# Performance work log

Measured on AMD Instinct MI355X. Metric: run time of the kernel, lower is better.

## Reference

```python
import jax, jax.numpy as jnp
import numpy as np

DIM = 2048


def setup_inputs() -> dict:
    key = jax.random.key(0)
    k1, k2 = jax.random.split(key)
    skew_kernel = jax.random.normal(k1, (DIM, DIM), dtype=jnp.float32) * 0.01
    dt = jax.random.uniform(k2, (8, 256), dtype=jnp.float32)  # [batch, time]
    return {"skew_kernel": skew_kernel, "dt": dt}


def reference(skew_kernel, dt):
    # Build strictly skew-symmetric A from the upper triangle of the kernel
    K = jnp.triu(skew_kernel, 1)
    A = K - K.T                                  # [dim, dim], A^T = -A
    # H = i*A is Hermitian -> real eigenvalues L_real, unitary V
    H = (1j * A).astype(jnp.complex64)
    L_real, V = jnp.linalg.eigh(H)               # L_real: [dim], V: [dim, dim]
    L = (-1j) * L_real.astype(jnp.complex64)     # purely imaginary spectrum of A
    V_inv = V.conj().T                           # unitary inverse
    # dt broadcasting per original: ndim==2 -> [..., None]; ndim==1 -> [-1,1,1]
    if dt.ndim == 2:
        dt_cast = dt[:, :, None]
    elif dt.ndim == 1:
        dt_cast = dt.reshape(-1, 1, 1)
    else:
        dt_cast = dt[..., None]
    evo_diag = jnp.exp(L[None, None, :] * dt_cast.astype(jnp.complex64))  # [B, T, dim]
    return V, V_inv, evo_diag
```

## Files before the change

kernel.cpp:

```cpp
#include <hip/hip_runtime.h>
#include <math.h>

#define DN 2048
#define LEAF 16
#define NLEAVES 128
#define NB 64
#define SPLITK 32
#define EPSF 5.9604645e-08f
#define SAFMINF 1.17549435e-38f

typedef float2 cplx;

struct Ctl {
  float orgnrm;
  int K;
  int ctot[4];
  float rho;
  int nrot;
  int n12, n23;
};

__device__ __forceinline__ cplx mkc(float x, float y){ cplx c; c.x=x; c.y=y; return c; }
__device__ __forceinline__ cplx cmul(cplx a, cplx b){ return mkc(a.x*b.x - a.y*b.y, a.x*b.y + a.y*b.x); }
__device__ __forceinline__ cplx cconj(cplx a){ return mkc(a.x, -a.y); }
__device__ __forceinline__ cplx cadd(cplx a, cplx b){ return mkc(a.x+b.x, a.y+b.y); }
__device__ __forceinline__ cplx cinv(cplx b){
  if (fabsf(b.x) >= fabsf(b.y)) { float r = b.y/b.x; float den = b.x + b.y*r; return mkc(1.f/den, -r/den); }
  else { float r = b.x/b.y; float den = b.x*r + b.y; return mkc(r/den, -1.f/den); }
}

__global__ void k_zeroCnt(int* cnt){ if (threadIdx.x==0) *cnt = 0; }

__global__ void k_buildH_t(const float* sk, cplx* AH){
  __shared__ float tA[32][33], tB[32][33];
  int C0 = blockIdx.x*32, R0 = blockIdx.y*32;
  int tx = threadIdx.x & 31, ty = threadIdx.x >> 5;
  for (int p=0;p<4;p++){
    int ry = ty + 8*p;
    tA[ry][tx] = sk[(size_t)(R0+ry)*DN + C0+tx];
    tB[ry][tx] = sk[(size_t)(C0+ry)*DN + R0+tx];
  }
  __syncthreads();
  for (int p=0;p<4;p++){
    int cy = ty + 8*p;
    int r = R0 + tx, c = C0 + cy;
    float im;
    if (r > c) im = -tB[cy][tx];
    else if (r < c) im = tA[tx][cy];
    else im = 0.f;
    AH[(size_t)c*DN + r] = mkc(copysignf(0.f, im), im);
  }
}

__global__ void k_gemv3(cplx* AH, cplx* wpart, float* ssqpart,
                        cplx* dp, cplx* pa, cplx* a0copy, cplx* scl,
                        cplx* tauA, float* e, int* cnt, int j, int m, int chunk){
  __shared__ float rx[256], ry[256];
  __shared__ int slast;
  __shared__ cplx s_ssc;
  __shared__ int s_do;
  int t = threadIdx.x;
  int b = blockIdx.x, s = blockIdx.y;
  int i = b*256 + t;
  cplx* colr = AH + (size_t)j*DN;
  cplx* x = colr + (j+2);
  int cc0 = s*chunk, cc1 = cc0+chunk; if (cc1 > m-1) cc1 = m-1;
  if (cc0 > m-1) cc0 = m-1;
  if (b == 0){
    float ss = 0.f;
    for (int cc = cc0+t; cc < cc1; cc += 256){ cplx v = x[cc]; ss += v.x*v.x + v.y*v.y; }
    rx[t] = ss; __syncthreads();
    for (int q=128;q>0;q>>=1){ if (t<q) rx[t]+=rx[t+q]; __syncthreads(); }
    if (t==0) ssqpart[s] = rx[0];
    __syncthreads();
  }
  cplx acc = mkc(0.f,0.f);
  if (i < m){
    for (int cc = cc0; cc < cc1; ++cc){
      cplx a = AH[(size_t)(j+2+cc)*DN + (j+1+i)];
      cplx v = x[cc];
      acc.x += a.x*v.x - a.y*v.y;
      acc.y += a.x*v.y + a.y*v.x;
    }
    wpart[(size_t)s*DN + i] = acc;
  }
  cplx a0v = mkc(0.f,0.f);
  if (s == 0 && i < m){
    a0v = AH[(size_t)(j+1)*DN + (j+1+i)];
    a0copy[i] = a0v;
  }
  {
    float dxx=0.f, dyy=0.f;
    if (i >= 1 && i < m){
      cplx xv = x[i-1];
      dxx = acc.x*xv.x + acc.y*xv.y;
      dyy = acc.x*xv.y - acc.y*xv.x;
    }
    rx[t]=dxx; ry[t]=dyy; __syncthreads();
    for (int q=128;q>0;q>>=1){ if (t<q){ rx[t]+=rx[t+q]; ry[t]+=ry[t+q]; } __syncthreads(); }
    if (t==0) dp[b*SPLITK + s] = mkc(rx[0], ry[0]);
    __syncthreads();
  }
  if (s == 0){
    float px=0.f, py=0.f;
    if (i >= 1 && i < m){
      cplx xv = x[i-1];
      px = a0v.x*xv.x + a0v.y*xv.y;
      py = a0v.x*xv.y - a0v.y*xv.x;
    }
    rx[t]=px; ry[t]=py; __syncthreads();
    for (int q=128;q>0;q>>=1){ if (t<q){ rx[t]+=rx[t+q]; ry[t]+=ry[t+q]; } __syncthreads(); }
    if (t==0) pa[b] = mkc(rx[0], ry[0]);
    __syncthreads();
  }
  __threadfence();
  if (t == 0){
    int total = gridDim.x * gridDim.y;
    int old = atomicAdd(cnt, 1);
    slast = (old == total-1) ? 1 : 0;
  }
  __syncthreads();
  if (!slast) return;
  __threadfence();
  int nb = gridDim.x;
  if (t == 0){
    *cnt = 0;
    float xn2 = 0.f;
    for (int q=0;q<SPLITK;q++) xn2 += ssqpart[q];
    cplx alpha = colr[j+1];
    if (sqrtf(xn2) == 0.f && alpha.y == 0.f){
      s_do = 0;
      tauA[j] = mkc(0.f,0.f); e[j] = alpha.x;
      scl[0] = mkc(0.f,0.f); scl[1] = mkc(0.f,0.f); scl[2] = mkc(0.f,0.f);
    } else {
      s_do = 1;
      float beta = -copysignf(sqrtf(alpha.x*alpha.x + alpha.y*alpha.y + xn2), alpha.x);
      cplx tj = mkc((beta - alpha.x)/beta, -alpha.y/beta);
      cplx ssc = cinv(mkc(alpha.x - beta, alpha.y));
      tauA[j] = tj; e[j] = beta;
      colr[j+1] = mkc(beta, 0.f);
      s_ssc = ssc;
      cplx P0 = mkc(0.f,0.f);
      for (int q=0;q<SPLITK;q++){ cplx u = wpart[(size_t)q*DN]; P0.x+=u.x; P0.y+=u.y; }
      cplx SP = mkc(0.f,0.f);
      for (int bb=0;bb<nb;bb++) for (int q=0;q<SPLITK;q++){ cplx u = dp[bb*SPLITK+q]; SP.x+=u.x; SP.y+=u.y; }
      cplx SA = mkc(0.f,0.f);
      for (int bb=0;bb<nb;bb++){ cplx u = pa[bb]; SA.x+=u.x; SA.y+=u.y; }
      cplx a0d = a0copy[0];
      cplx T1 = cadd(cconj(a0d), cmul(ssc, SA));
      cplx T2 = cadd(cconj(P0), cmul(ssc, SP));
      cplx dot = cmul(cconj(tj), cadd(T1, cmul(cconj(ssc), T2)));
      cplx td = cmul(tj, dot);
      scl[0] = tj; scl[1] = ssc; scl[2] = mkc(-td.x, 0.f);
    }
  }
  __syncthreads();
  if (s_do){
    cplx ssc = s_ssc;
    for (int r=j+2+t; r<DN; r+=256) colr[r] = cmul(colr[r], ssc);
  }
}

__global__ void k_her2w(cplx* AH, const cplx* wpart, const cplx* a0copy,
                        const cplx* scl, int j, int m){
  __shared__ cplx wr[32], wcs[16];
  int t = threadIdx.x;
  cplx tj = scl[0], ssc = scl[1];
  float a2 = scl[2].x;
  int r0 = blockIdx.x*32, c0 = blockIdx.y*16;
  if (t < 48){
    int idx = (t < 32) ? (r0 + t) : (c0 + (t-32));
    cplx wv = mkc(0.f,0.f);
    if (idx < m){
      cplx P = mkc(0.f,0.f);
      for (int s=0;s<SPLITK;s++){ cplx u = wpart[(size_t)s*DN + idx]; P.x+=u.x; P.y+=u.y; }
      cplx av = cadd(a0copy[idx], cmul(ssc, P));
      wv = cmul(tj, av);
    }
    if (t < 32) wr[t] = wv; else wcs[t-32] = wv;
  }
  __syncthreads();
  int r = r0 + (t & 31);
  int cb = c0 + (t >> 5)*2;
  if (r >= m) return;
  const cplx* vcol = AH + (size_t)j*DN + (j+1);
  cplx vr = (r==0)? mkc(1.f,0.f) : vcol[r];
  cplx wrv = wr[t & 31];
  for (int c = cb; c < cb+2; ++c){
    if (c >= m) break;
    cplx vc = (c==0)? mkc(1.f,0.f) : vcol[c];
    cplx wcv = wcs[c - c0];
    cplx u1 = cmul(vr, cconj(wcv));
    cplx u2 = cmul(wrv, cconj(vc));
    cplx u3 = cmul(vr, cconj(vc));
    size_t idx = (size_t)(j+1+c)*DN + (j+1+r);
    AH[idx].x -= u1.x + u2.x + a2*u3.x;
    AH[idx].y -= u1.y + u2.y + a2*u3.y;
  }
}

__global__ void k_collectD(const cplx* AH, float* d){
  int i = blockIdx.x*256 + threadIdx.x;
  if (i < DN) d[i] = AH[(size_t)i*DN + i].x;
}

__global__ void k_zeroZ(float* Z){
  int idx = blockIdx.x*256 + threadIdx.x;
  if (idx < DN*DN) Z[idx] = 0.f;
}

__global__ void k_predc(float* d, float* e, int* indxq, Ctl* ctl){
  __shared__ float red[256];
  int t = threadIdx.x;
  float mx = 0.f;
  for (int i=t;i<DN;i+=256) mx = fmaxf(mx, fabsf(d[i]));
  for (int i=t;i<DN-1;i+=256) mx = fmaxf(mx, fabsf(e[i]));
  red[t]=mx; __syncthreads();
  for (int s=128;s>0;s>>=1){ if (t<s) red[t]=fmaxf(red[t],red[t+s]); __syncthreads(); }
  float orgnrm = red[0];
  if (t==0) ctl->orgnrm = orgnrm;
  float mul = 1.f/orgnrm;
  __syncthreads();
  for (int i=t;i<DN;i+=256) d[i]*=mul;
  for (int i=t;i<DN-1;i+=256) e[i]*=mul;
  __syncthreads();
  if (t==0){
    for (int b=1;b<NLEAVES;b++){ int s0=b*LEAF; float ae=fabsf(e[s0-1]); d[s0-1]-=ae; d[s0]-=ae; }
  }
  for (int i=t;i<DN;i+=256) indxq[i] = (i & (LEAF-1)) + 1;
}

__device__ void slaev2_d(float a, float b, float c, float* rt1, float* rt2, float* cs1, float* sn1){
  float sm = a + c, df = a - c, adf = fabsf(df), tb = b + b, ab = fabsf(tb);
  float acmx, acmn;
  if (fabsf(a) > fabsf(c)) { acmx = a; acmn = c; } else { acmx = c; acmn = a; }
  float rt;
  if (adf > ab) rt = adf*sqrtf(1.f + (ab/adf)*(ab/adf));
  else if (adf < ab) rt = ab*sqrtf(1.f + (adf/ab)*(adf/ab));
  else rt = ab*sqrtf(2.f);
  int sgn1;
  if (sm < 0.f){ *rt1 = 0.5f*(sm - rt); sgn1 = -1; *rt2 = (acmx/(*rt1))*acmn - (b/(*rt1))*b; }
  else if (sm > 0.f){ *rt1 = 0.5f*(sm + rt); sgn1 = 1; *rt2 = (acmx/(*rt1))*acmn - (b/(*rt1))*b; }
  else { *rt1 = 0.5f*rt; *rt2 = -0.5f*rt; sgn1 = 1; }
  float cs; int sgn2;
  if (df >= 0.f){ cs = df + rt; sgn2 = 1; } else { cs = df - rt; sgn2 = -1; }
  float acs = fabsf(cs);
  if (acs > ab){ float ct = -tb/cs; *sn1 = 1.f/sqrtf(1.f + ct*ct); *cs1 = ct*(*sn1); }
  else {
    if (ab == 0.f){ *cs1 = 1.f; *sn1 = 0.f; }
    else { float tn = -cs/tb; *cs1 = 1.f/sqrtf(1.f + tn*tn); *sn1 = tn*(*cs1); }
  }
  if (sgn1 == sgn2){ float tn = *cs1; *cs1 = -(*sn1); *sn1 = tn; }
}

__device__ void slartg_d(float f, float g, float* cs, float* sn, float* r){
  if (g == 0.f){ *cs = 1.f; *sn = 0.f; *r = f; }
  else if (f == 0.f){ *cs = 0.f; *sn = copysignf(1.f, g); *r = fabsf(g); }
  else {
    float d = sqrtf(f*f + g*g);
    *cs = fabsf(f)/d;
    *r = copysignf(d, f);
    *sn = g/(*r);
  }
}

__device__ void rot1_d(float* z, int ldz, int nr, int col, float cc, float ss){
  for (int r=0;r<nr;++r){
    float tmp = z[(col+1)*ldz + r];
    z[(col+1)*ldz + r] = cc*tmp - ss*z[col*ldz + r];
    z[col*ldz + r] = ss*tmp + cc*z[col*ldz + r];
  }
}

__device__ void ssteqr_small(int n, float* d, float* e, float* z, int ldz){
  for (int c=0;c<n;c++) for (int r=0;r<n;r++) z[c*ldz+r] = (r==c)?1.f:0.f;
  const float eps=EPSF, eps2=eps*eps, safmin=SAFMINF;
  int nmaxit = n*30, jtot=0;
  int l1=0;
  float wc[LEAF], ws_[LEAF];
  while (1){
    if (l1 > n-1) break;
    if (l1 > 0) e[l1-1] = 0.f;
    int m;
    for (m = l1; m <= n-2; ++m){
      float tst = fabsf(e[m]);
      if (tst == 0.f) break;
// ... 382 lines not shown
  if (j >= K) return;
  int t = threadIdx.x;
  float* col = Zmat + (size_t)(off+j)*DN + off;
  float ssq = 0.f;
  for (int i=t;i<K;i+=256){
    float den = col[i];
    if (den == 0.f) den = 1e-30f;
    float v = what[off+i]/den; sv[i]=v; ssq += v*v;
  }
  red[t]=ssq; __syncthreads();
  for (int s=128;s>0;s>>=1){ if (t<s) red[t]+=red[t+s]; __syncthreads(); }
  float temp = sqrtf(red[0]);
  for (int i=t;i<K;i+=256) col[i] = sv[indxc[off+i]]/temp;
}

__global__ void k_mcopyS_b(float* Smatg, const float* Zmat, const Ctl* ctls, int n, int mode){
  int q = blockIdx.y;
  int off = q*n;
  const Ctl* ctl = ctls + q;
  int K = ctl->K; if (K==0) return;
  int rows = (mode==1)? ctl->n23 : ctl->n12;
  int rowoff = (mode==1)? ctl->ctot[0] : 0;
  if (rows==0) return;
  float* Smat = Smatg + (size_t)off*n;
  size_t tot = (size_t)rows*K;
  for (size_t idx = (size_t)blockIdx.x*256+threadIdx.x; idx < tot; idx += (size_t)gridDim.x*256){
    int r = (int)(idx % rows); int c = (int)(idx / rows);
    Smat[idx] = Zmat[(size_t)(off+c)*DN + off + rowoff + r];
  }
}

__global__ void k_sgemm_dc64_b(float* Zmat, const float* Q2g, const float* Smatg,
                               const Ctl* ctls, int n, int mode){
  int q = blockIdx.z;
  int off = q*n;
  const Ctl* ctl = ctls + q;
  int K = ctl->K; if (K==0) return;
  int n1 = n/2, n2 = n-n1;
  const float* Q2 = Q2g + (size_t)off*n;
  const float* Smat = Smatg + (size_t)off*n;
  int m, kd; const float* A; int lda; float* C;
  if (mode==1){ m=n2; kd=ctl->n23; A = Q2 + (size_t)n1*ctl->n12; lda=n2; C = Zmat + (size_t)off*DN + off+n1; }
  else { m=n1; kd=ctl->n12; A = Q2; lda=n1; C = Zmat + (size_t)off*DN + off; }
  int tr = blockIdx.x*64, tc = blockIdx.y*64;
  if (tr >= m || tc >= K) return;
  __shared__ float As[64][17], Bs[16][65];
  int tid = threadIdx.x, tx = tid & 15, ty = tid >> 4;
  float acc[4][4];
  #pragma unroll
  for (int i=0;i<4;i++) for (int jq=0;jq<4;jq++) acc[i][jq]=0.f;
  for (int k0=0;k0<kd;k0+=16){
    #pragma unroll
    for (int p=0;p<4;p++){
      int r = tid & 63, kk = (tid >> 6) + 4*p;
      As[r][kk] = (tr+r<m && k0+kk<kd) ? A[(size_t)(k0+kk)*lda + tr+r] : 0.f;
    }
    #pragma unroll
    for (int p=0;p<4;p++){
      int kk = tid & 15, c = (tid >> 4) + 16*p;
      Bs[kk][c] = (k0+kk<kd && tc+c<K) ? Smat[(size_t)(tc+c)*kd + k0+kk] : 0.f;
    }
    __syncthreads();
    #pragma unroll
    for (int k=0;k<16;k++){
      float a[4], b[4];
      #pragma unroll
      for (int i=0;i<4;i++){ a[i]=As[tx+16*i][k]; b[i]=Bs[k][ty+16*i]; }
      #pragma unroll
      for (int i=0;i<4;i++)
        #pragma unroll
        for (int jq=0;jq<4;jq++) acc[i][jq] += a[i]*b[jq];
    }
    __syncthreads();
  }
  #pragma unroll
  for (int i=0;i<4;i++)
    #pragma unroll
    for (int jq=0;jq<4;jq++){
      int r = tr+tx+16*i, c = tc+ty+16*jq;
      if (r < m && c < K) C[(size_t)c*DN + r] = acc[i][jq];
    }
}

__global__ void k_mmerge_b(float* d, int* indxq, const Ctl* ctls, int n){
  int q = blockIdx.x;
  int off = q*n;
  int K = ctls[q].K;
  if (K == 0){ for (int i=0;i<n;i++) indxq[off+i]=i+1; return; }
  int i1=0, i2=n-1, ns1=K, ns2=n-K, k=0;
  while (ns1>0 && ns2>0){
    if (d[off+i1] <= d[off+i2]){ indxq[off+k++]=i1+1; i1++; ns1--; }
    else { indxq[off+k++]=i2+1; i2--; ns2--; }
  }
  while (ns1>0){ indxq[off+k++]=i1+1; i1++; ns1--; }
  while (ns2>0){ indxq[off+k++]=i2+1; i2--; ns2--; }
}

__global__ void k_fpermA(const float* d, const float* Zmat, float* Q2, float* dtmp, const int* indxq){
  int i = blockIdx.x; int t = threadIdx.x;
  int src = indxq[i]-1;
  if (t==0) dtmp[i] = d[src];
  const float* sc = Zmat + (size_t)src*DN;
  float* dc = Q2 + (size_t)i*DN;
  for (int r=t;r<DN;r+=256) dc[r]=sc[r];
}
__global__ void k_fpermB(float* evals, float* Zmat, const float* Q2, const float* dtmp, const Ctl* ctl){
  int i = blockIdx.x; int t = threadIdx.x;
  if (t==0) evals[i] = dtmp[i]*ctl->orgnrm;
  const float* sc = Q2 + (size_t)i*DN;
  float* dc = Zmat + (size_t)i*DN;
  for (int r=t;r<DN;r+=256) dc[r]=sc[r];
}

__global__ void k_packV(const cplx* AH, cplx* Vp, int i0, int ib, int m){
  int idx = blockIdx.x*256 + threadIdx.x;
  if (idx >= m*ib) return;
  int r = idx % m, c = idx / m;
  int grow = i0+1+r, pc = i0+c+1;
  cplx v;
  if (grow < pc) v = mkc(0.f,0.f);
  else if (grow == pc) v = mkc(1.f,0.f);
  else v = AH[(size_t)(i0+c)*DN + grow];
  Vp[(size_t)c*m + r] = v;
}

__global__ void k_vhv(const cplx* Vp, cplx* vhv, int m, int ib){
  __shared__ float rx[256], ry[256];
  int c = blockIdx.x; if (c >= ib) return;
  int t = threadIdx.x;
  for (int r=0; r<c; ++r){
    float dx=0.f, dy=0.f;
    for (int rl=c+t; rl<m; rl+=256){
      cplx a = Vp[(size_t)r*m + rl];
      cplx b = Vp[(size_t)c*m + rl];
      dx += a.x*b.x + a.y*b.y;
      dy += a.x*b.y - a.y*b.x;
    }
    rx[t]=dx; ry[t]=dy; __syncthreads();
    for (int s=128;s>0;s>>=1){ if (t<s){ rx[t]+=rx[t+s]; ry[t]+=ry[t+s]; } __syncthreads(); }
    if (t==0) vhv[r + c*NB] = mkc(rx[0], ry[0]);
    __syncthreads();
  }
}

__global__ void k_bldT(const cplx* vhv, const cplx* tau, cplx* T, int ib){
  int t = threadIdx.x;
  for (int idx=t; idx<NB*NB; idx+=64) T[idx] = mkc(0.f,0.f);
  __syncthreads();
  for (int c=0; c<ib; ++c){
    if (t < c){
      cplx acc = mkc(0.f,0.f);
      for (int q=t; q<c; ++q) acc = cadd(acc, cmul(T[t + q*NB], vhv[q + c*NB]));
      cplx nt = mkc(-tau[c].x, -tau[c].y);
      T[t + c*NB] = cmul(nt, acc);
    }
    if (t == c) T[c + c*NB] = tau[c];
    __syncthreads();
  }
}

__global__ void k_cgemm_ct64(const cplx* A, const float* Cre, const float* Cim,
                             cplx* G1, int row0, int m, int ib, int ksz){
  int tc = blockIdx.y*64;
  int s = blockIdx.z;
  int ks0 = s*ksz, ks1 = ks0 + ksz; if (ks1 > m) ks1 = m;
  __shared__ cplx As[64][17], Bs[16][65];
  int tid = threadIdx.x, tx = tid & 15, ty = tid >> 4;
  cplx acc[4][4];
  #pragma unroll
  for (int i=0;i<4;i++) for (int jq=0;jq<4;jq++) acc[i][jq]=mkc(0.f,0.f);
  for (int k0 = ks0; k0 < ks1; k0 += 16){
    #pragma unroll
    for (int p=0;p<4;p++){
      int kk = tid & 15, r = (tid >> 4) + 16*p;
      cplx v = mkc(0.f,0.f);
      if (r < ib && k0+kk < ks1) v = cconj(A[(size_t)r*m + k0+kk]);
      As[r][kk] = v;
    }
    #pragma unroll
    for (int p=0;p<4;p++){
      int kk = tid & 15, c = (tid >> 4) + 16*p;
      cplx v = mkc(0.f,0.f);
      int kg = k0+kk, cg = tc+c;
      if (kg < ks1 && cg < DN){ size_t bi = (size_t)cg*DN + row0 + kg; v = mkc(Cre[bi], Cim[bi]); }
      Bs[kk][c] = v;
    }
    __syncthreads();
    #pragma unroll
    for (int k=0;k<16;k++){
      cplx a[4], b[4];
      #pragma unroll
      for (int i=0;i<4;i++){ a[i]=As[tx+16*i][k]; b[i]=Bs[k][ty+16*i]; }
      #pragma unroll
      for (int i=0;i<4;i++)
        #pragma unroll
        for (int jq=0;jq<4;jq++){
          acc[i][jq].x += a[i].x*b[jq].x - a[i].y*b[jq].y;
          acc[i][jq].y += a[i].x*b[jq].y + a[i].y*b[jq].x;
        }
    }
    __syncthreads();
  }
  #pragma unroll
  for (int i=0;i<4;i++)
    #pragma unroll
    for (int jq=0;jq<4;jq++){
      int r = tx+16*i, c = tc+ty+16*jq;
      if (r < ib && c < DN) G1[(size_t)s*NB*DN + r + (size_t)c*NB] = acc[i][jq];
    }
}

__global__ void k_cgemm_nn(const cplx* A, int lda, const cplx* B, int ldb,
                           cplx* C, int ldc, int m, int nn, int kk, int S, int ssz){
  __shared__ cplx As[32][33], Bs[32][33];
  int tr = blockIdx.x*32, tc = blockIdx.y*32;
  if (tr >= m || tc >= nn) return;
  int tx = threadIdx.x & 31, ty = threadIdx.x >> 5;
  cplx acc[4]; for (int q=0;q<4;q++) acc[q]=mkc(0.f,0.f);
  for (int k0=0;k0<kk;k0+=32){
    for (int q=0;q<4;q++){ int kc=k0+ty+q*8; int r=tr+tx;
      As[tx][ty+q*8] = (r<m && kc<kk)? A[(size_t)kc*lda + r] : mkc(0.f,0.f); }
    for (int q=0;q<4;q++){ int cc=tc+ty+q*8; int kr=k0+tx;
      cplx v = mkc(0.f,0.f);
      if (kr<kk && cc<nn){
        for (int s=0;s<S;s++){ cplx u = B[(size_t)s*ssz + kr + (size_t)cc*ldb]; v.x+=u.x; v.y+=u.y; }
// ... 42 lines not shown
    for (int k=0;k<16;k++){
      cplx a[4], b[4];
      #pragma unroll
      for (int i=0;i<4;i++){ a[i]=As[tx+16*i][k]; b[i]=Bs[k][ty+16*i]; }
      #pragma unroll
      for (int i=0;i<4;i++)
        #pragma unroll
        for (int jq=0;jq<4;jq++){
          acc[i][jq].x += a[i].x*b[jq].x - a[i].y*b[jq].y;
          acc[i][jq].y += a[i].x*b[jq].y + a[i].y*b[jq].x;
        }
    }
    __syncthreads();
  }
  #pragma unroll
  for (int i=0;i<4;i++)
    #pragma unroll
    for (int jq=0;jq<4;jq++){
      int r = tr+tx+16*i, c = tc+ty+16*jq;
      if (r < m && c < DN){
        size_t idx = (size_t)c*DN + row0 + r;
        Cre[idx] -= acc[i][jq].x;
        Cim[idx] -= acc[i][jq].y;
      }
    }
}

__global__ void k_outVre_t(const float* Cre, float* out0){
  __shared__ float tile[32][33];
  int C0 = blockIdx.x*32, R0 = blockIdx.y*32;
  int tx = threadIdx.x & 31, ty = threadIdx.x >> 5;
  for (int p=0;p<4;p++){
    int cy = ty + 8*p;
    tile[cy][tx] = Cre[(size_t)(C0+cy)*DN + R0+tx];
  }
  __syncthreads();
  for (int p=0;p<4;p++){
    int ry = ty + 8*p;
    out0[(size_t)(R0+ry)*DN + C0+tx] = tile[tx][ry];
  }
}
__global__ void k_outVinv(const float* Cre, float* out1){
  int idx = blockIdx.x*256 + threadIdx.x;
  if (idx >= DN*DN) return;
  out1[idx] = Cre[idx];
}
__global__ void k_outEvo(const float* evals, const float* dt, float* out2, int T){
  int idx = blockIdx.x*256 + threadIdx.x;
  if (idx >= T*DN) return;
  int k = idx & (DN-1), tt = idx >> 11;
  out2[idx] = cosf(evals[k]*dt[tt]);
}

extern "C" void kernel_launch(void* const* d_in, const int* in_sizes, int n_in,
                              void* d_out, int out_size, void* d_ws, size_t ws_size,
                              hipStream_t stream)
{
  const float* sk = (const float*)d_in[0];
  const float* dt = (const float*)d_in[1];
  int Ttot = in_sizes[1];
  float* out = (float*)d_out;
  (void)n_in; (void)out_size;

  const size_t N2 = (size_t)DN*DN;
  cplx*  AH   = (cplx*)out;
  float* Smat = out + 2*N2;
  float* Zmat = (float*)d_ws;
  float* Q2   = (float*)d_ws + N2;
  float* Cre  = Zmat;
  float* Cim  = Q2;

  char* wp = (char*)d_ws + 2*N2*sizeof(float);
  auto carve = [&](size_t b)->void*{ void* p=(void*)wp; wp += (b+255)&~(size_t)255; return p; };
  float* dd     = (float*)carve(DN*sizeof(float));
  float* ee     = (float*)carve(DN*sizeof(float));
  float* dtmp   = (float*)carve(DN*sizeof(float));
  float* dlamda = (float*)carve(DN*sizeof(float));
  float* wkeep  = (float*)carve(DN*sizeof(float));
  float* what   = (float*)carve(DN*sizeof(float));
  float* dgrp   = (float*)carve(DN*sizeof(float));
  float* rotc   = (float*)carve(DN*sizeof(float));
  float* rots   = (float*)carve(DN*sizeof(float));
  float* evals  = (float*)carve(DN*sizeof(float));
  float* ssqpart= (float*)carve(64*sizeof(float));
  cplx*  tauA   = (cplx*)carve(DN*sizeof(cplx));
  cplx*  a0copy = (cplx*)carve(DN*sizeof(cplx));
  cplx*  dp     = (cplx*)carve(512*sizeof(cplx));
  cplx*  pa     = (cplx*)carve(64*sizeof(cplx));
  cplx*  scl    = (cplx*)carve(8*sizeof(cplx));
  int*   cnt    = (int*)carve(16*sizeof(int));
  int*   indxq  = (int*)carve(DN*sizeof(int));
  int*   indx   = (int*)carve(DN*sizeof(int));
  int*   indxc  = (int*)carve(DN*sizeof(int));
  int*   rotp   = (int*)carve(DN*sizeof(int));
  int*   rotn   = (int*)carve(DN*sizeof(int));
  Ctl*   ctlG   = (Ctl*)carve(sizeof(Ctl));
  Ctl*   ctls   = (Ctl*)carve(NLEAVES*sizeof(Ctl));
  cplx*  Vp     = (cplx*)carve((size_t)DN*NB*sizeof(cplx));
  cplx*  G2     = (cplx*)carve((size_t)NB*DN*sizeof(cplx));
  cplx*  Tm     = (cplx*)carve((size_t)NB*NB*sizeof(cplx));
  cplx*  vhv    = (cplx*)carve((size_t)NB*NB*sizeof(cplx));
  size_t used = (size_t)(wp - (char*)d_ws);
  int S = 8;
  while (S > 1 && (ws_size != 0) && (used + (size_t)S*NB*DN*sizeof(cplx) > ws_size)) S >>= 1;
  if (ws_size == 0) S = 1;
  cplx*  G1     = (cplx*)carve((size_t)S*NB*DN*sizeof(cplx));
  cplx*  wpart  = Vp;

  k_zeroCnt<<<1,1,0,stream>>>(cnt);

  {
    dim3 gb(DN/32, DN/32);
    k_buildH_t<<<gb,256,0,stream>>>(sk, AH);
  }

  for (int j=0; j<=DN-2; ++j){
    int m = DN-1-j;
    int chunk = (m-1 + SPLITK - 1)/SPLITK;
    dim3 gv((m+255)/256, SPLITK);
    k_gemv3<<<gv,256,0,stream>>>(AH, wpart, ssqpart, dp, pa, a0copy, scl, tauA, ee, cnt, j, m, chunk);
    dim3 g2((m+31)/32,(m+15)/16);
    k_her2w<<<g2,256,0,stream>>>(AH, wpart, a0copy, scl, j, m);
  }
  k_collectD<<<(DN+255)/256,256,0,stream>>>(AH, dd);

  k_zeroZ<<<(DN*DN+255)/256,256,0,stream>>>(Zmat);
  k_predc<<<1,256,0,stream>>>(dd, ee, indxq, ctlG);
  k_leaves<<<NLEAVES,64,0,stream>>>(dd, ee, Zmat);

  for (int szv = LEAF; szv < DN; szv *= 2){
    int n = 2*szv;
    int M = DN/n;
    k_mprep_b<<<M,256,0,stream>>>(dd, ee, Zmat, indxq, dlamda, wkeep, indx, indxc,
                                  rotc, rots, rotp, rotn, ctls, n);
    k_mrot_b<<<dim3((n+255)/256, M),256,0,stream>>>(Zmat, rotc, rots, rotp, rotn, ctls, n);
    k_mcopyA_b<<<dim3(n, M),256,0,stream>>>(dd, Zmat, Q2, dgrp, indx, ctls, n);
    k_mcopyB_b<<<dim3(n, M),256,0,stream>>>(dd, Zmat, Q2, dgrp, ctls, n);
    k_msec_b<<<dim3((n+63)/64, M),64,0,stream>>>(dd, Zmat, dlamda, wkeep, ctls, n);
    k_mzhat_b<<<dim3((n+63)/64, M),64,0,stream>>>(dlamda, wkeep, what, Zmat, ctls, n);
    k_mvec_b<<<dim3(n, M),256,0,stream>>>(Zmat, what, indxc, ctls, n);
    int gcs = ((n*n)+255)/256; if (gcs > 4096) gcs = 4096;
    k_mcopyS_b<<<dim3(gcs, M),256,0,stream>>>(Smat, Zmat, ctls, n, 1);
    dim3 gg((n+63)/64,(n+63)/64,M);
    k_sgemm_dc64_b<<<gg,256,0,stream>>>(Zmat, Q2, Smat, ctls, n, 1);
    k_mcopyS_b<<<dim3(gcs, M),256,0,stream>>>(Smat, Zmat, ctls, n, 2);
    k_sgemm_dc64_b<<<gg,256,0,stream>>>(Zmat, Q2, Smat, ctls, n, 2);
    k_mmerge_b<<<M,1,0,stream>>>(dd, indxq, ctls, n);
  }
  k_fpermA<<<DN,256,0,stream>>>(dd, Zmat, Q2, dtmp, indxq);
  k_fpermB<<<DN,256,0,stream>>>(evals, Zmat, Q2, dtmp, ctlG);

  k_outEvo<<<((Ttot*DN)+255)/256,256,0,stream>>>(evals, dt, out + 2*N2, Ttot);

  k_zeroZ<<<(DN*DN+255)/256,256,0,stream>>>(Cim);
  int Krefl = DN-1;
  for (int i0 = ((Krefl-1)/NB)*NB; i0 >= 0; i0 -= NB){
    int ib = Krefl - i0; if (ib > NB) ib = NB;
    int m = DN-1-i0;
    int row0 = i0+1;
    k_packV<<<((m*ib)+255)/256,256,0,stream>>>(AH, Vp, i0, ib, m);
    k_vhv<<<ib,256,0,stream>>>(Vp, vhv, m, ib);
    k_bldT<<<1,64,0,stream>>>(vhv, tauA+i0, Tm, ib);
    int ksz = ((m + S - 1)/S + 15) & ~15;
    dim3 gct(1, DN/64, S);
    k_cgemm_ct64<<<gct,256,0,stream>>>(Vp, Cre, Cim, G1, row0, m, ib, ksz);
    dim3 gnn((ib+31)/32, (DN+31)/32);
    k_cgemm_nn<<<gnn,256,0,stream>>>(Tm, NB, G1, NB, G2, NB, ib, DN, ib, S, NB*DN);
    dim3 gup((m+63)/64, DN/64);
    k_cupdate64<<<gup,256,0,stream>>>(Vp, G2, Cre, Cim, row0, m, ib);
  }

  {
    dim3 gt(DN/32, DN/32);
    k_outVre_t<<<gt,256,0,stream>>>(Cre, out);
  }
  k_outVinv<<<(DN*DN+255)/256,256,0,stream>>>(Cre, out + N2);
}
```

Measured before the change: 133.1 ms.

## Fuse Householder tridiagonalization loop into one persistent cooperative kernel

New measurement: 419.1 ms. +214.9%, slower.

```diff
diff --git a/kernel.cpp b/kernel.cpp
--- a/kernel.cpp
+++ b/kernel.cpp
@@ -1,11 +1,15 @@
 #include <hip/hip_runtime.h>
+#include <hip/hip_cooperative_groups.h>
 #include <math.h>
+
+namespace cg = cooperative_groups;
 
 #define DN 2048
 #define LEAF 16
 #define NLEAVES 128
 #define NB 64
-#define SPLITK 32
+#define CSK 64
+#define GBLK 512
 #define EPSF 5.9604645e-08f
 #define SAFMINF 1.17549435e-38f
 
@@ -29,8 +33,6 @@
   else { float r = b.x/b.y; float den = b.x*r + b.y; return mkc(r/den, -1.f/den); }
 }
 
-__global__ void k_zeroCnt(int* cnt){ if (threadIdx.x==0) *cnt = 0; }
-
 __global__ void k_buildH_t(const float* sk, cplx* AH){
   __shared__ float tA[32][33], tB[32][33];
   int C0 = blockIdx.x*32, R0 = blockIdx.y*32;
@@ -52,156 +54,174 @@
   }
 }
 
-__global__ void k_gemv3(cplx* AH, cplx* wpart, float* ssqpart,
-                        cplx* dp, cplx* pa, cplx* a0copy, cplx* scl,
-                        cplx* tauA, float* e, int* cnt, int j, int m, int chunk){
+__global__ void __launch_bounds__(256) k_chetd2(
+    cplx* AH, cplx* wpart, float* ssqpart, cplx* dp, cplx* pa,
+    cplx* a0copy, cplx* wvec, cplx* tauA, float* e, float* d)
+{
+  cg::grid_group gg = cg::this_grid();
   __shared__ float rx[256], ry[256];
-  __shared__ int slast;
-  __shared__ cplx s_ssc;
-  __shared__ int s_do;
+  __shared__ float sb_[16];
   int t = threadIdx.x;
-  int b = blockIdx.x, s = blockIdx.y;
-  int i = b*256 + t;
-  cplx* colr = AH + (size_t)j*DN;
-  cplx* x = colr + (j+2);
-  int cc0 = s*chunk, cc1 = cc0+chunk; if (cc1 > m-1) cc1 = m-1;
-  if (cc0 > m-1) cc0 = m-1;
-  if (b == 0){
-    float ss = 0.f;
-    for (int cc = cc0+t; cc < cc1; cc += 256){ cplx v = x[cc]; ss += v.x*v.x + v.y*v.y; }
-    rx[t] = ss; __syncthreads();
-    for (int q=128;q>0;q>>=1){ if (t<q) rx[t]+=rx[t+q]; __syncthreads(); }
-    if (t==0) ssqpart[s] = rx[0];
-    __syncthreads();
-  }
-  cplx acc = mkc(0.f,0.f);
-  if (i < m){
-    for (int cc = cc0; cc < cc1; ++cc){
-      cplx a = AH[(size_t)(j+2+cc)*DN + (j+1+i)];
-      cplx v = x[cc];
-      acc.x += a.x*v.x - a.y*v.y;
-      acc.y += a.x*v.y + a.y*v.x;
-    }
-    wpart[(size_t)s*DN + i] = acc;
-  }
-  cplx a0v = mkc(0.f,0.f);
-  if (s == 0 && i < m){
-    a0v = AH[(size_t)(j+1)*DN + (j+1+i)];
-    a0copy[i] = a0v;
-  }
-  {
-    float dxx=0.f, dyy=0.f;
-    if (i >= 1 && i < m){
-      cplx xv = x[i-1];
-      dxx = acc.x*xv.x + acc.y*xv.y;
-      dyy = acc.x*xv.y - acc.y*xv.x;
-    }
-    rx[t]=dxx; ry[t]=dyy; __syncthreads();
-    for (int q=128;q>0;q>>=1){ if (t<q){ rx[t]+=rx[t+q]; ry[t]+=ry[t+q]; } __syncthreads(); }
-    if (t==0) dp[b*SPLITK + s] = mkc(rx[0], ry[0]);
-    __syncthreads();
-  }
-  if (s == 0){
-    float px=0.f, py=0.f;
-    if (i >= 1 && i < m){
-      cplx xv = x[i-1];
-      px = a0v.x*xv.x + a0v.y*xv.y;
-      py = a0v.x*xv.y - a0v.y*xv.x;
-    }
-    rx[t]=px; ry[t]=py; __syncthreads();
-    for (int q=128;q>0;q>>=1){ if (t<q){ rx[t]+=rx[t+q]; ry[t]+=ry[t+q]; } __syncthreads(); }
-    if (t==0) pa[b] = mkc(rx[0], ry[0]);
-    __syncthreads();
-  }
-  __threadfence();
-  if (t == 0){
-    int total = gridDim.x * gridDim.y;
-    int old = atomicAdd(cnt, 1);
-    slast = (old == total-1) ? 1 : 0;
-  }
-  __syncthreads();
-  if (!slast) return;
-  __threadfence();
-  int nb = gridDim.x;
-  if (t == 0){
-    *cnt = 0;
-    float xn2 = 0.f;
-    for (int q=0;q<SPLITK;q++) xn2 += ssqpart[q];
-    cplx alpha = colr[j+1];
-    if (sqrtf(xn2) == 0.f && alpha.y == 0.f){
-      s_do = 0;
-      tauA[j] = mkc(0.f,0.f); e[j] = alpha.x;
-      scl[0] = mkc(0.f,0.f); scl[1] = mkc(0.f,0.f); scl[2] = mkc(0.f,0.f);
-    } else {
-      s_do = 1;
-      float beta = -copysignf(sqrtf(alpha.x*alpha.x + alpha.y*alpha.y + xn2), alpha.x);
-      cplx tj = mkc((beta - alpha.x)/beta, -alpha.y/beta);
-      cplx ssc = cinv(mkc(alpha.x - beta, alpha.y));
-      tauA[j] = tj; e[j] = beta;
-      colr[j+1] = mkc(beta, 0.f);
-      s_ssc = ssc;
-      cplx P0 = mkc(0.f,0.f);
-      for (int q=0;q<SPLITK;q++){ cplx u = wpart[(size_t)q*DN]; P0.x+=u.x; P0.y+=u.y; }
-      cplx SP = mkc(0.f,0.f);
-      for (int bb=0;bb<nb;bb++) for (int q=0;q<SPLITK;q++){ cplx u = dp[bb*SPLITK+q]; SP.x+=u.x; SP.y+=u.y; }
-      cplx SA = mkc(0.f,0.f);
-      for (int bb=0;bb<nb;bb++){ cplx u = pa[bb]; SA.x+=u.x; SA.y+=u.y; }
-      cplx a0d = a0copy[0];
-      cplx T1 = cadd(cconj(a0d), cmul(ssc, SA));
-      cplx T2 = cadd(cconj(P0), cmul(ssc, SP));
-      cplx dot = cmul(cconj(tj), cadd(T1, cmul(cconj(ssc), T2)));
-      cplx td = cmul(tj, dot);
-      scl[0] = tj; scl[1] = ssc; scl[2] = mkc(-td.x, 0.f);
-    }
-  }
-  __syncthreads();
-  if (s_do){
-    cplx ssc = s_ssc;
-    for (int r=j+2+t; r<DN; r+=256) colr[r] = cmul(colr[r], ssc);
-  }
-}
-
-__global__ void k_her2w(cplx* AH, const cplx* wpart, const cplx* a0copy,
-                        const cplx* scl, int j, int m){
-  __shared__ cplx wr[32], wcs[16];
-  int t = threadIdx.x;
-  cplx tj = scl[0], ssc = scl[1];
-  float a2 = scl[2].x;
-  int r0 = blockIdx.x*32, c0 = blockIdx.y*16;
-  if (t < 48){
-    int idx = (t < 32) ? (r0 + t) : (c0 + (t-32));
-    cplx wv = mkc(0.f,0.f);
-    if (idx < m){
-      cplx P = mkc(0.f,0.f);
-      for (int s=0;s<SPLITK;s++){ cplx u = wpart[(size_t)s*DN + idx]; P.x+=u.x; P.y+=u.y; }
-      cplx av = cadd(a0copy[idx], cmul(ssc, P));
-      wv = cmul(tj, av);
-    }
-    if (t < 32) wr[t] = wv; else wcs[t-32] = wv;
-  }
-  __syncthreads();
-  int r = r0 + (t & 31);
-  int cb = c0 + (t >> 5)*2;
-  if (r >= m) return;
-  const cplx* vcol = AH + (size_t)j*DN + (j+1);
-  cplx vr = (r==0)? mkc(1.f,0.f) : vcol[r];
-  cplx wrv = wr[t & 31];
-  for (int c = cb; c < cb+2; ++c){
-    if (c >= m) break;
-    cplx vc = (c==0)? mkc(1.f,0.f) : vcol[c];
-    cplx wcv = wcs[c - c0];
-    cplx u1 = cmul(vr, cconj(wcv));
-    cplx u2 = cmul(wrv, cconj(vc));
-    cplx u3 = cmul(vr, cconj(vc));
-    size_t idx = (size_t)(j+1+c)*DN + (j+1+r);
-    AH[idx].x -= u1.x + u2.x + a2*u3.x;
-    AH[idx].y -= u1.y + u2.y + a2*u3.y;
-  }
-}
-
-__global__ void k_collectD(const cplx* AH, float* d){
-  int i = blockIdx.x*256 + threadIdx.x;
-  if (i < DN) d[i] = AH[(size_t)i*DN + i].x;
+  int bid = blockIdx.x, G = gridDim.x;
+
+  for (int j = 0; j <= DN-2; ++j){
+    int m = DN-1-j;
+    int nb = (m+255)/256;
+    int chunk = (m-1 + CSK-1)/CSK;
+    cplx* colr = AH + (size_t)j*DN;
+    cplx* x = colr + (j+2);
+
+    for (int tt = bid; tt < nb*CSK; tt += G){
+      int b = tt / CSK, s = tt - b*CSK;
+      int cc0 = s*chunk, cc1 = cc0+chunk;
+      if (cc1 > m-1) cc1 = m-1;
+      if (cc0 > m-1) cc0 = m-1;
+      int i = b*256 + t;
+      if (b == 0){
+        float ss = 0.f;
+        for (int cc = cc0+t; cc < cc1; cc += 256){ cplx v = x[cc]; ss += v.x*v.x + v.y*v.y; }
+        __syncthreads();
+        rx[t] = ss; __syncthreads();
+        for (int q=128;q>0;q>>=1){ if (t<q) rx[t]+=rx[t+q]; __syncthreads(); }
+        if (t==0) ssqpart[s] = rx[0];
+      }
+      cplx acc = mkc(0.f,0.f);
+      if (i < m){
+        for (int cc = cc0; cc < cc1; ++cc){
+          cplx a = AH[(size_t)(j+2+cc)*DN + (j+1+i)];
+          cplx v = x[cc];
+          acc.x += a.x*v.x - a.y*v.y;
+          acc.y += a.x*v.y + a.y*v.x;
+        }
+        wpart[(size_t)s*DN + i] = acc;
+      }
+      cplx a0v = mkc(0.f,0.f);
+      if (s == 0 && i < m){
+        a0v = AH[(size_t)(j+1)*DN + (j+1+i)];
+        a0copy[i] = a0v;
+      }
+      float dxx=0.f, dyy=0.f;
+      if (i >= 1 && i < m){
+        cplx xv = x[i-1];
+        dxx = acc.x*xv.x + acc.y*xv.y;
+        dyy = acc.x*xv.y - acc.y*xv.x;
+      }
+      __syncthreads();
+      rx[t]=dxx; ry[t]=dyy; __syncthreads();
+      for (int q=128;q>0;q>>=1){ if (t<q){ rx[t]+=rx[t+q]; ry[t]+=ry[t+q]; } __syncthreads(); }
+      if (t==0) dp[b*CSK + s] = mkc(rx[0], ry[0]);
+      if (s == 0){
+        float px=0.f, py=0.f;
+        if (i >= 1 && i < m){
+          cplx xv = x[i-1];
+          px = a0v.x*xv.x + a0v.y*xv.y;
+          py = a0v.x*xv.y - a0v.y*xv.x;
+        }
+        __syncthreads();
+        rx[t]=px; ry[t]=py; __syncthreads();
+        for (int q=128;q>0;q>>=1){ if (t<q){ rx[t]+=rx[t+q]; ry[t]+=ry[t+q]; } __syncthreads(); }
+        if (t==0) pa[b] = mkc(rx[0], ry[0]);
+      }
+    }
+    gg.sync();
+
+    {
+      __syncthreads();
+      rx[t] = (t < CSK) ? ssqpart[t] : 0.f;
+      __syncthreads();
+      for (int q=128;q>0;q>>=1){ if (t<q) rx[t]+=rx[t+q]; __syncthreads(); }
+      if (t==0) sb_[8] = rx[0];
+      __syncthreads();
+      float spx=0.f, spy=0.f;
+      for (int idx=t; idx<nb*CSK; idx+=256){ cplx u = dp[idx]; spx+=u.x; spy+=u.y; }
+      rx[t]=spx; ry[t]=spy; __syncthreads();
+      for (int q=128;q>0;q>>=1){ if (t<q){ rx[t]+=rx[t+q]; ry[t]+=ry[t+q]; } __syncthreads(); }
+      if (t==0){ sb_[9]=rx[0]; sb_[10]=ry[0]; }
+      __syncthreads();
+      rx[t] = (t<nb)? pa[t].x : 0.f; ry[t] = (t<nb)? pa[t].y : 0.f;
+      __syncthreads();
+      for (int q=128;q>0;q>>=1){ if (t<q){ rx[t]+=rx[t+q]; ry[t]+=ry[t+q]; } __syncthreads(); }
+      if (t==0){ sb_[11]=rx[0]; sb_[12]=ry[0]; }
+      __syncthreads();
+      rx[t] = (t<CSK)? wpart[(size_t)t*DN].x : 0.f;
+      ry[t] = (t<CSK)? wpart[(size_t)t*DN].y : 0.f;
+      __syncthreads();
+      for (int q=128;q>0;q>>=1){ if (t<q){ rx[t]+=rx[t+q]; ry[t]+=ry[t+q]; } __syncthreads(); }
+      if (t==0){
+        float xn2 = sb_[8];
+        cplx SP = mkc(sb_[9], sb_[10]);
+        cplx SA = mkc(sb_[11], sb_[12]);
+        cplx P0 = mkc(rx[0], ry[0]);
+        cplx alpha = colr[j+1];
+        if (sqrtf(xn2) == 0.f && alpha.y == 0.f){
+          sb_[6] = 0.f; sb_[0]=0.f; sb_[1]=0.f; sb_[2]=0.f; sb_[3]=0.f; sb_[4]=0.f; sb_[5]=0.f;
+          sb_[7] = alpha.x;
+        } else {
+          float beta = -copysignf(sqrtf(alpha.x*alpha.x + alpha.y*alpha.y + xn2), alpha.x);
+          cplx tj = mkc((beta - alpha.x)/beta, -alpha.y/beta);
+          cplx ssc = cinv(mkc(alpha.x - beta, alpha.y));
+          cplx a0d = a0copy[0];
+          cplx T1 = cadd(cconj(a0d), cmul(ssc, SA));
+          cplx T2 = cadd(cconj(P0), cmul(ssc, SP));
+          cplx dot = cmul(cconj(tj), cadd(T1, cmul(cconj(ssc), T2)));
+          cplx td = cmul(tj, dot);
+          sb_[0]=tj.x; sb_[1]=tj.y; sb_[2]=ssc.x; sb_[3]=ssc.y;
+          sb_[4]=-0.5f*td.x; sb_[5]=-0.5f*td.y;
+          sb_[6]=1.f; sb_[7]=beta;
+        }
+      }
+      __syncthreads();
+      int sdo = (sb_[6] != 0.f);
+      cplx tj = mkc(sb_[0], sb_[1]);
+      cplx ssc = mkc(sb_[2], sb_[3]);
+      cplx al = mkc(sb_[4], sb_[5]);
+      float beta = sb_[7];
+      for (int i = bid*256 + t; i < m; i += G*256){
+        if (sdo){
+          cplx P = mkc(0.f,0.f);
+          #pragma unroll 8
+          for (int s=0;s<CSK;s++){ cplx u = wpart[(size_t)s*DN + i]; P.x+=u.x; P.y+=u.y; }
+          cplx av = cadd(a0copy[i], cmul(ssc, P));
+          cplx w1 = cmul(tj, av);
+          cplx vi;
+          if (i == 0){ vi = mkc(1.f,0.f); colr[j+1] = mkc(beta, 0.f); }
+          else { vi = cmul(ssc, colr[j+1+i]); colr[j+1+i] = vi; }
+          wvec[i] = cadd(w1, cmul(al, vi));
+        } else {
+          wvec[i] = mkc(0.f,0.f);
+        }
+      }
+      if (bid == 0 && t == 0){
+        if (sdo){ e[j] = beta; tauA[j] = tj; }
+        else { e[j] = sb_[7]; tauA[j] = mkc(0.f,0.f); }
+      }
+    }
+    gg.sync();
+
+    if (sb_[6] != 0.f){
+      int ntr = (m+31)/32, ntc = (m+15)/16;
+      const cplx* vcol = colr + (j+1);
+      for (int tt = bid; tt < ntr*ntc; tt += G){
+        int trb = tt % ntr, tcb = tt / ntr;
+        int r = trb*32 + (t & 31);
+        int cb = tcb*16 + ((t >> 5)*2);
+        if (r < m){
+          cplx vr = (r==0)? mkc(1.f,0.f) : vcol[r];
+          cplx wr = wvec[r];
+          for (int c = cb; c < cb+2; ++c){
+            if (c >= m) break;
+            cplx vc = (c==0)? mkc(1.f,0.f) : vcol[c];
+            cplx wc = wvec[c];
+            cplx u = cadd(cmul(vr, cconj(wc)), cmul(wr, cconj(vc)));
+            size_t idx = (size_t)(j+1+c)*DN + (j+1+r);
+            AH[idx].x -= u.x; AH[idx].y -= u.y;
+          }
+        }
+      }
+    }
+    gg.sync();
+  }
+  for (int i = bid*256 + t; i < DN; i += G*256) d[i] = AH[(size_t)i*DN + i].x;
 }
 
 __global__ void k_zeroZ(float* Z){
@@ -792,23 +812,21 @@
   Vp[(size_t)c*m + r] = v;
 }
 
-__global__ void k_vhv(const cplx* Vp, cplx* vhv, int m, int ib){
+__global__ void k_vhv2(const cplx* Vp, cplx* vhv, int m, int ib){
   __shared__ float rx[256], ry[256];
-  int c = blockIdx.x; if (c >= ib) return;
+  int r = blockIdx.x, c = blockIdx.y;
+  if (r >= c || c >= ib) return;
   int t = threadIdx.x;
-  for (int r=0; r<c; ++r){
-    float dx=0.f, dy=0.f;
-    for (int rl=c+t; rl<m; rl+=256){
-      cplx a = Vp[(size_t)r*m + rl];
-      cplx b = Vp[(size_t)c*m + rl];
-      dx += a.x*b.x + a.y*b.y;
-      dy += a.x*b.y - a.y*b.x;
-    }
-    rx[t]=dx; ry[t]=dy; __syncthreads();
-    for (int s=128;s>0;s>>=1){ if (t<s){ rx[t]+=rx[t+s]; ry[t]+=ry[t+s]; } __syncthreads(); }
-    if (t==0) vhv[r + c*NB] = mkc(rx[0], ry[0]);
-    __syncthreads();
-  }
+  float dx=0.f, dy=0.f;
+  for (int rl=c+t; rl<m; rl+=256){
+    cplx a = Vp[(size_t)r*m + rl];
+    cplx b = Vp[(size_t)c*m + rl];
+    dx += a.x*b.x + a.y*b.y;
+    dy += a.x*b.y - a.y*b.x;
+  }
+  rx[t]=dx; ry[t]=dy; __syncthreads();
+  for (int s=128;s>0;s>>=1){ if (t<s){ rx[t]+=rx[t+s]; ry[t]+=ry[t+s]; } __syncthreads(); }
+  if (t==0) vhv[r + c*NB] = mkc(rx[0], ry[0]);
 }
 
 __global__ void k_bldT(const cplx* vhv, const cplx* tau, cplx* T, int ib){
@@ -1017,13 +1035,12 @@
   float* rotc   = (float*)carve(DN*sizeof(float));
   float* rots   = (float*)carve(DN*sizeof(float));
   float* evals  = (float*)carve(DN*sizeof(float));
-  float* ssqpart= (float*)carve(64*sizeof(float));
+  float* ssqpart= (float*)carve(CSK*sizeof(float));
   cplx*  tauA   = (cplx*)carve(DN*sizeof(cplx));
   cplx*  a0copy = (cplx*)carve(DN*sizeof(cplx));
-  cplx*  dp     = (cplx*)carve(512*sizeof(cplx));
+  cplx*  wvecA  = (cplx*)carve(DN*sizeof(cplx));
+  cplx*  dp     = (cplx*)carve(8*CSK*sizeof(cplx));
   cplx*  pa     = (cplx*)carve(64*sizeof(cplx));
-  cplx*  scl    = (cplx*)carve(8*sizeof(cplx));
-  int*   cnt    = (int*)carve(16*sizeof(int));
   int*   indxq  = (int*)carve(DN*sizeof(int));
   int*   indx   = (int*)carve(DN*sizeof(int));
   int*   indxc  = (int*)carve(DN*sizeof(int));
@@ -1042,22 +1059,16 @@
   cplx*  G1     = (cplx*)carve((size_t)S*NB*DN*sizeof(cplx));
   cplx*  wpart  = Vp;
 
-  k_zeroCnt<<<1,1,0,stream>>>(cnt);
-
   {
     dim3 gb(DN/32, DN/32);
     k_buildH_t<<<gb,256,0,stream>>>(sk, AH);
   }
 
-  for (int j=0; j<=DN-2; ++j){
-    int m = DN-1-j;
-    int chunk = (m-1 + SPLITK - 1)/SPLITK;
-    dim3 gv((m+255)/256, SPLITK);
-    k_gemv3<<<gv,256,0,stream>>>(AH, wpart, ssqpart, dp, pa, a0copy, scl, tauA, ee, cnt, j, m, chunk);
-    dim3 g2((m+31)/32,(m+15)/16);
-    k_her2w<<<g2,256,0,stream>>>(AH, wpart, a0copy, scl, j, m);
-  }
-  k_collectD<<<(DN+255)/256,256,0,stream>>>(AH, dd);
+  {
+    void* kargs[] = { (void*)&AH, (void*)&wpart, (void*)&ssqpart, (void*)&dp, (void*)&pa,
+                      (void*)&a0copy, (void*)&wvecA, (void*)&tauA, (void*)&ee, (void*)&dd };
+    hipLaunchCooperativeKernel((void*)k_chetd2, dim3(GBLK), dim3(256), kargs, 0, stream);
+  }
 
   k_zeroZ<<<(DN*DN+255)/256,256,0,stream>>>(Zmat);
   k_predc<<<1,256,0,stream>>>(dd, ee, indxq, ctlG);
@@ -1094,7 +1105,8 @@
     int m = DN-1-i0;
     int row0 = i0+1;
     k_packV<<<((m*ib)+255)/256,256,0,stream>>>(AH, Vp, i0, ib, m);
-    k_vhv<<<ib,256,0,stream>>>(Vp, vhv, m, ib);
+    dim3 gvh(ib, ib);
+    k_vhv2<<<gvh,256,0,stream>>>(Vp, vhv, m, ib);
     k_bldT<<<1,64,0,stream>>>(vhv, tauA+i0, Tm, ib);
     int ksz = ((m + S - 1)/S + 15) & ~15;
     dim3 gct(1, DN/64, S);
```

## Enlarge her2 tiles, parallelize merge via shared memory, and 2D-grid vhv dots

Applied to the files above, without the earlier changes.

New measurement: 130.1 ms. 2.2% less time.

```diff
diff --git a/kernel.cpp b/kernel.cpp
--- a/kernel.cpp
+++ b/kernel.cpp
@@ -161,41 +161,58 @@
   }
 }
 
-__global__ void k_her2w(cplx* AH, const cplx* wpart, const cplx* a0copy,
+__global__ void __launch_bounds__(256) k_her2w(cplx* AH, const cplx* wpart, const cplx* a0copy,
                         const cplx* scl, int j, int m){
-  __shared__ cplx wr[32], wcs[16];
+  __shared__ cplx wsh[128];
+  __shared__ cplx vsh[128];
+  __shared__ cplx part[256];
   int t = threadIdx.x;
+  int r0 = blockIdx.x*64, c0 = blockIdx.y*64;
   cplx tj = scl[0], ssc = scl[1];
   float a2 = scl[2].x;
-  int r0 = blockIdx.x*32, c0 = blockIdx.y*16;
-  if (t < 48){
-    int idx = (t < 32) ? (r0 + t) : (c0 + (t-32));
-    cplx wv = mkc(0.f,0.f);
-    if (idx < m){
-      cplx P = mkc(0.f,0.f);
-      for (int s=0;s<SPLITK;s++){ cplx u = wpart[(size_t)s*DN + idx]; P.x+=u.x; P.y+=u.y; }
-      cplx av = cadd(a0copy[idx], cmul(ssc, P));
+  const cplx* vcol = AH + (size_t)j*DN + (j+1);
+  {
+    int idx = t >> 1;
+    int half = t & 1;
+    int gi = (idx < 64) ? (r0 + idx) : (c0 + (idx-64));
+    cplx P = mkc(0.f,0.f);
+    if (gi < m){
+      int s0 = half*(SPLITK/2);
+      for (int s=s0; s<s0+(SPLITK/2); ++s){ cplx u = wpart[(size_t)s*DN + gi]; P.x+=u.x; P.y+=u.y; }
+    }
+    part[t] = P;
+  }
+  __syncthreads();
+  if (t < 128){
+    int gi = (t < 64) ? (r0 + t) : (c0 + (t-64));
+    cplx wv = mkc(0.f,0.f), vv = mkc(0.f,0.f);
+    if (gi < m){
+      cplx P = cadd(part[2*t], part[2*t+1]);
+      cplx av = cadd(a0copy[gi], cmul(ssc, P));
       wv = cmul(tj, av);
-    }
-    if (t < 32) wr[t] = wv; else wcs[t-32] = wv;
-  }
-  __syncthreads();
-  int r = r0 + (t & 31);
-  int cb = c0 + (t >> 5)*2;
-  if (r >= m) return;
-  const cplx* vcol = AH + (size_t)j*DN + (j+1);
-  cplx vr = (r==0)? mkc(1.f,0.f) : vcol[r];
-  cplx wrv = wr[t & 31];
-  for (int c = cb; c < cb+2; ++c){
-    if (c >= m) break;
-    cplx vc = (c==0)? mkc(1.f,0.f) : vcol[c];
-    cplx wcv = wcs[c - c0];
-    cplx u1 = cmul(vr, cconj(wcv));
-    cplx u2 = cmul(wrv, cconj(vc));
-    cplx u3 = cmul(vr, cconj(vc));
-    size_t idx = (size_t)(j+1+c)*DN + (j+1+r);
-    AH[idx].x -= u1.x + u2.x + a2*u3.x;
-    AH[idx].y -= u1.y + u2.y + a2*u3.y;
+      vv = (gi==0)? mkc(1.f,0.f) : vcol[gi];
+    }
+    wsh[t] = wv; vsh[t] = vv;
+  }
+  __syncthreads();
+  int rl = t & 15, cl = t >> 4;
+  #pragma unroll
+  for (int q=0;q<4;q++){
+    int c = c0 + cl + 16*q;
+    if (c >= m) continue;
+    cplx vc = vsh[64 + cl + 16*q], wc = wsh[64 + cl + 16*q];
+    #pragma unroll
+    for (int i=0;i<4;i++){
+      int r = r0 + rl + 16*i;
+      if (r >= m) continue;
+      cplx vr = vsh[rl + 16*i], wr = wsh[rl + 16*i];
+      cplx u1 = cmul(vr, cconj(wc));
+      cplx u2 = cmul(wr, cconj(vc));
+      cplx u3 = cmul(vr, cconj(vc));
+      size_t idx2 = (size_t)(j+1+c)*DN + (j+1+r);
+      AH[idx2].x -= u1.x + u2.x + a2*u3.x;
+      AH[idx2].y -= u1.y + u2.y + a2*u3.y;
+    }
   }
 }
 
@@ -750,18 +767,30 @@
     }
 }
 
-__global__ void k_mmerge_b(float* d, int* indxq, const Ctl* ctls, int n){
+__global__ void __launch_bounds__(256) k_mmerge_b(float* d, int* indxq, const Ctl* ctls, int n){
+  __shared__ float sd[2048];
+  __shared__ int sq[2048];
   int q = blockIdx.x;
   int off = q*n;
+  int t = threadIdx.x;
   int K = ctls[q].K;
-  if (K == 0){ for (int i=0;i<n;i++) indxq[off+i]=i+1; return; }
-  int i1=0, i2=n-1, ns1=K, ns2=n-K, k=0;
-  while (ns1>0 && ns2>0){
-    if (d[off+i1] <= d[off+i2]){ indxq[off+k++]=i1+1; i1++; ns1--; }
-    else { indxq[off+k++]=i2+1; i2--; ns2--; }
-  }
-  while (ns1>0){ indxq[off+k++]=i1+1; i1++; ns1--; }
-  while (ns2>0){ indxq[off+k++]=i2+1; i2--; ns2--; }
+  if (K == 0){
+    for (int i=t;i<n;i+=256) indxq[off+i] = i+1;
+    return;
+  }
+  for (int i=t;i<n;i+=256) sd[i] = d[off+i];
+  __syncthreads();
+  if (t == 0){
+    int i1=0, i2=n-1, ns1=K, ns2=n-K, k=0;
+    while (ns1>0 && ns2>0){
+      if (sd[i1] <= sd[i2]){ sq[k++]=i1+1; i1++; ns1--; }
+      else { sq[k++]=i2+1; i2--; ns2--; }
+    }
+    while (ns1>0){ sq[k++]=i1+1; i1++; ns1--; }
+    while (ns2>0){ sq[k++]=i2+1; i2--; ns2--; }
+  }
+  __syncthreads();
+  for (int i=t;i<n;i+=256) indxq[off+i] = sq[i];
 }
 
 __global__ void k_fpermA(const float* d, const float* Zmat, float* Q2, float* dtmp, const int* indxq){
@@ -792,23 +821,21 @@
   Vp[(size_t)c*m + r] = v;
 }
 
-__global__ void k_vhv(const cplx* Vp, cplx* vhv, int m, int ib){
+__global__ void k_vhv2(const cplx* Vp, cplx* vhv, int m, int ib){
   __shared__ float rx[256], ry[256];
-  int c = blockIdx.x; if (c >= ib) return;
+  int r = blockIdx.x, c = blockIdx.y;
+  if (r >= c || c >= ib) return;
   int t = threadIdx.x;
-  for (int r=0; r<c; ++r){
-    float dx=0.f, dy=0.f;
-    for (int rl=c+t; rl<m; rl+=256){
-      cplx a = Vp[(size_t)r*m + rl];
-      cplx b = Vp[(size_t)c*m + rl];
-      dx += a.x*b.x + a.y*b.y;
-      dy += a.x*b.y - a.y*b.x;
-    }
-    rx[t]=dx; ry[t]=dy; __syncthreads();
-    for (int s=128;s>0;s>>=1){ if (t<s){ rx[t]+=rx[t+s]; ry[t]+=ry[t+s]; } __syncthreads(); }
-    if (t==0) vhv[r + c*NB] = mkc(rx[0], ry[0]);
-    __syncthreads();
-  }
+  float dx=0.f, dy=0.f;
+  for (int rl=c+t; rl<m; rl+=256){
+    cplx a = Vp[(size_t)r*m + rl];
+    cplx b = Vp[(size_t)c*m + rl];
+    dx += a.x*b.x + a.y*b.y;
+    dy += a.x*b.y - a.y*b.x;
+  }
+  rx[t]=dx; ry[t]=dy; __syncthreads();
+  for (int s=128;s>0;s>>=1){ if (t<s){ rx[t]+=rx[t+s]; ry[t]+=ry[t+s]; } __syncthreads(); }
+  if (t==0) vhv[r + c*NB] = mkc(rx[0], ry[0]);
 }
 
 __global__ void k_bldT(const cplx* vhv, const cplx* tau, cplx* T, int ib){
@@ -1054,7 +1081,7 @@
     int chunk = (m-1 + SPLITK - 1)/SPLITK;
     dim3 gv((m+255)/256, SPLITK);
     k_gemv3<<<gv,256,0,stream>>>(AH, wpart, ssqpart, dp, pa, a0copy, scl, tauA, ee, cnt, j, m, chunk);
-    dim3 g2((m+31)/32,(m+15)/16);
+    dim3 g2((m+63)/64,(m+63)/64);
     k_her2w<<<g2,256,0,stream>>>(AH, wpart, a0copy, scl, j, m);
   }
   k_collectD<<<(DN+255)/256,256,0,stream>>>(AH, dd);
@@ -1080,7 +1107,7 @@
     k_sgemm_dc64_b<<<gg,256,0,stream>>>(Zmat, Q2, Smat, ctls, n, 1);
     k_mcopyS_b<<<dim3(gcs, M),256,0,stream>>>(Smat, Zmat, ctls, n, 2);
     k_sgemm_dc64_b<<<gg,256,0,stream>>>(Zmat, Q2, Smat, ctls, n, 2);
-    k_mmerge_b<<<M,1,0,stream>>>(dd, indxq, ctls, n);
+    k_mmerge_b<<<M,256,0,stream>>>(dd, indxq, ctls, n);
   }
   k_fpermA<<<DN,256,0,stream>>>(dd, Zmat, Q2, dtmp, indxq);
   k_fpermB<<<DN,256,0,stream>>>(evals, Zmat, Q2, dtmp, ctlG);
@@ -1094,7 +1121,8 @@
     int m = DN-1-i0;
     int row0 = i0+1;
     k_packV<<<((m*ib)+255)/256,256,0,stream>>>(AH, Vp, i0, ib, m);
-    k_vhv<<<ib,256,0,stream>>>(Vp, vhv, m, ib);
+    dim3 gvh(ib, ib);
+    k_vhv2<<<gvh,256,0,stream>>>(Vp, vhv, m, ib);
     k_bldT<<<1,64,0,stream>>>(vhv, tauA+i0, Tm, ib);
     int ksz = ((m + S - 1)/S + 15) & ~15;
     dim3 gct(1, DN/64, S);
```
